# Kernel optimization log

Hardware: AMD Instinct MI355X
Metric: run time of the kernel (lower is better)

## Reference

```python
import jax, jax.numpy as jnp
import numpy as np

BLOCK_SIZE = 32
NUM_PROJS = 7


def _unit_hamming(n):
    # AngularLSH._unit_hamming_distance_array (Gray-code-like permutation)
    a = np.array([0, 1], dtype=np.int32)
    for i in range(1, n):
        a = np.concatenate([a, a[::-1] + 2 ** i])
    return a


def _lsh_hash(x, proj_dir, perm, enc_vec):
    # x: [B,H,N,D], proj_dir: [1,1,D,P] -> hash ids [B,H,N]
    pd = proj_dir[0, 0]  # [D,P]
    proj = jnp.einsum('bhnd,dp->bhnp', x, pd)
    bits = (proj > 0).astype(jnp.int32)
    bin_ids = (bits * enc_vec).sum(-1)
    return perm[bin_ids]


def _causal_attn(q, k, v):
    # q,k,v: [B,N,H,D] (xformers layout), causal softmax attention
    B, N, H, D = q.shape
    s = jnp.einsum('bqhd,bkhd->bhqk', q, k) * (D ** -0.5)
    causal = jnp.tril(jnp.ones((N, N), dtype=bool))
    s = jnp.where(causal, s, jnp.finfo(s.dtype).min)
    w = jax.nn.softmax(s, axis=-1)
    return jnp.einsum('bhqk,bkhd->bqhd', w, v)


def _forward(q, k, v, proj_dir):
    B, N, H, D = q.shape
    bs = BLOCK_SIZE
    nb = N // bs
    perm = jnp.asarray(_unit_hamming(NUM_PROJS))
    enc_vec = jnp.asarray(2 ** np.arange(NUM_PROJS, dtype=np.int32))

    qt = jnp.transpose(q, (0, 2, 1, 3))  # [B,H,N,D]
    kt = jnp.transpose(k, (0, 2, 1, 3))

    q_hash = _lsh_hash(qt, proj_dir, perm, enc_vec)  # [B,H,N]
    sort_idx = jnp.argsort(q_hash, axis=2, stable=True)
    q_hash_sort = jnp.take_along_axis(q_hash, sort_idx, axis=2)
    inv_idx = jnp.argsort(sort_idx, axis=2, stable=True)
    q_sorted = jnp.take_along_axis(qt, sort_idx[..., None], axis=2)  # [B,H,N,D]

    k_hash = _lsh_hash(kt, proj_dir, perm, enc_vec)  # [B,H,N]

    # torch .view(seq_len, -1) on [B,H,N] contiguous tensors (C-order reshape)
    qh_rows = q_hash_sort.reshape(N, -1)  # [N, B*H]
    kh_rows = k_hash.reshape(N, -1)
    eq = (qh_rows == kh_rows).reshape(nb, -1)  # rows grouped by query block
    keep = (eq.sum(axis=1) > 0)  # [nb] block kept if any hash match

    # K_split_per_block = k.reshape(B, nb, -1, D) on [B,H,N,D]
    k_blocks = kt.reshape(B, nb, (H * N) // nb, D)
    k_blocks = k_blocks * keep[None, :, None, None].astype(kt.dtype)
    k_crit = k_blocks.reshape(B, H, N, D)

    # out_critical = attn(q_critical, k_critical, v_critical) then unsort
    out = _causal_attn(jnp.transpose(q_sorted, (0, 2, 1, 3)),
                       jnp.transpose(k_crit, (0, 2, 1, 3)),
                       v)  # [B,N,H,D]
    out = jnp.take_along_axis(jnp.transpose(out, (0, 2, 1, 3)), inv_idx[..., None], axis=2)
    return jnp.transpose(out, (0, 2, 1, 3))  # [B,N,H,D]


def setup_inputs() -> dict:
    key = jax.random.key(0)
    k1, k2, k3, k4 = jax.random.split(key, 4)
    B, N, H, D = 2, 2048, 16, 128
    return {
        'q': jax.random.normal(k1, (B, N, H, D), dtype=jnp.float32),
        'k': jax.random.normal(k2, (B, N, H, D), dtype=jnp.float32),
        'v': jax.random.normal(k3, (B, N, H, D), dtype=jnp.float32),
        'proj_dir': jax.random.normal(k4, (1, 1, D, NUM_PROJS), dtype=jnp.float32),
        'is_causal': 1,
        'mask': jnp.zeros((1, 1), dtype=bool),
    }


def reference(q, k, v, proj_dir, is_causal, mask):
    # is_causal is always True at every attention call site; mask is unused then.
    return _forward(q, k, v, proj_dir)
```

## Files before the change

### kernel.cpp

```cpp
#include <hip/hip_runtime.h>
#include <cstdint>

#define BB 2
#define NN 2048
#define HH 16
#define DD 128
#define BH 32
#define NPROJ 7

typedef __bf16 bf16x8 __attribute__((ext_vector_type(8)));
typedef float f32x4 __attribute__((ext_vector_type(4)));

__device__ __forceinline__ unsigned short f2bf(float f) {
  unsigned int u = __float_as_uint(f);
  u += 0x7fff + ((u >> 16) & 1);
  return (unsigned short)(u >> 16);
}

__device__ __forceinline__ bf16x8 load_q8(const float* p) {
  float4 a = *(const float4*)p;
  float4 b = *(const float4*)(p + 4);
  unsigned short r[8] = {f2bf(a.x), f2bf(a.y), f2bf(a.z), f2bf(a.w),
                         f2bf(b.x), f2bf(b.y), f2bf(b.z), f2bf(b.w)};
  return *(bf16x8*)r;
}

__global__ void prep_kernel(const float* __restrict__ q, const float* __restrict__ k,
                            const float* __restrict__ v, const float* __restrict__ pd,
                            int* __restrict__ qh, int* __restrict__ kh,
                            unsigned short* __restrict__ Vt) {
  __shared__ __align__(16) char smem[64 * 132 * 2];
  if (blockIdx.x < 4096) {
    float* spd = (float*)smem;
    for (int i = threadIdx.x; i < DD * NPROJ; i += 256) spd[i] = pd[i];
    __syncthreads();
    long long gid = (long long)blockIdx.x * 256 + threadIdx.x;
    int part = (int)(gid & 7);
    long long row = gid >> 3;
    const long long NR = (long long)BB * NN * HH;
    int isk = row >= NR;
    long long r = isk ? row - NR : row;
    const float* src = (isk ? k : q) + r * DD + part * 16;
    double acc[NPROJ];
    for (int p = 0; p < NPROJ; ++p) acc[p] = 0.0;
    for (int d = 0; d < 16; d += 4) {
      float4 x = *(const float4*)(src + d);
      int dbase = part * 16 + d;
      for (int p = 0; p < NPROJ; ++p) {
        acc[p] += (double)x.x * (double)spd[(dbase + 0) * NPROJ + p]
                + (double)x.y * (double)spd[(dbase + 1) * NPROJ + p]
                + (double)x.z * (double)spd[(dbase + 2) * NPROJ + p]
                + (double)x.w * (double)spd[(dbase + 3) * NPROJ + p];
      }
    }
    for (int off = 1; off < 8; off <<= 1)
      for (int p = 0; p < NPROJ; ++p) acc[p] += __shfl_xor(acc[p], off);
    if (part == 0) {
      int bin = 0;
      for (int p = 0; p < NPROJ; ++p) bin |= ((int)(acc[p] > 0.0)) << p;
      int hsh = bin ^ (bin >> 1);
      int b_ = (int)(r / (NN * HH));
      int rem = (int)(r % (NN * HH));
      int n_ = rem / HH, h_ = rem % HH;
      (isk ? kh : qh)[((long long)b_ * HH + h_) * NN + n_] = hsh;
    }
  } else {
    unsigned short (*tile)[132] = (unsigned short(*)[132])smem;
    int blk = blockIdx.x - 4096;
    int bh = blk >> 5;
    int n0 = (blk & 31) * 64;
    int b = bh >> 4, h = bh & 15;
    for (int it = 0; it < 8; ++it) {
      int cid = it * 256 + threadIdx.x;
      int r = cid >> 5, d4 = (cid & 31) * 4;
      float4 x = *(const float4*)(v + (((long long)(b * NN + n0 + r) * HH + h) << 7) + d4);
      *(ushort4*)&tile[r][d4] = make_ushort4(f2bf(x.x), f2bf(x.y), f2bf(x.z), f2bf(x.w));
    }
    __syncthreads();
    for (int it = 0; it < 8; ++it) {
      int cid = it * 256 + threadIdx.x;
      int d = cid >> 4, n4 = (cid & 15) * 4;
      ushort4 y = make_ushort4(tile[n4 + 0][d], tile[n4 + 1][d], tile[n4 + 2][d], tile[n4 + 3][d]);
      *(ushort4*)(Vt + ((long long)bh * DD + d) * NN + n0 + n4) = y;
    }
  }
}

__global__ void sortkeep_kernel(const int* __restrict__ qh, const int* __restrict__ kh,
                                int* __restrict__ sidx, int* __restrict__ keep) {
  __shared__ int sh[NN];
  __shared__ int cnt[4][128];
  __shared__ int cum[128];
  __shared__ int kflag[2];
  int bh = blockIdx.x;
  const int* src = qh + (long long)bh * NN;
  for (int i = threadIdx.x; i < NN; i += 512) sh[i] = src[i];
  if (threadIdx.x < 2) kflag[threadIdx.x] = 0;
  __syncthreads();
  int bin = threadIdx.x & 127, seg = threadIdx.x >> 7;
  int n0 = seg * (NN / 4);
  int c = 0;
  for (int n = n0; n < n0 + NN / 4; ++n) c += (sh[n] == bin);
  cnt[seg][bin] = c;
  __syncthreads();
  if (threadIdx.x == 0) {
    int run = 0;
    for (int t = 0; t < 128; ++t) {
      cum[t] = run;
      run += cnt[0][t] + cnt[1][t] + cnt[2][t] + cnt[3][t];
    }
  }
  __syncthreads();
  int pos = cum[bin];
  for (int s = 0; s < seg; ++s) pos += cnt[s][bin];
  int f0 = 0, f1 = 0;
  for (int n = n0; n < n0 + NN / 4; ++n)
    if (sh[n] == bin) {
      sidx[(long long)bh * NN + pos] = n;
      int match = (bin == kh[(long long)bh * NN + pos]);
      if (pos < 1024) f0 |= match; else f1 |= match;
      ++pos;
    }
  if (f0) atomicOr(&kflag[0], 1);
  if (f1) atomicOr(&kflag[1], 1);
  __syncthreads();
  if (threadIdx.x < 2) keep[bh * 2 + threadIdx.x] = kflag[threadIdx.x];
}

__global__ __launch_bounds__(256, 1)
void flash_kernel(const float* __restrict__ q, const float* __restrict__ k,
                  const unsigned short* __restrict__ Vt, const int* __restrict__ sidx,
                  const int* __restrict__ keep, float* __restrict__ out) {
  __shared__ __align__(16) unsigned short Kt[64 * 136];
  __shared__ __align__(16) unsigned short Vs[128 * 72];
  __shared__ __align__(16) unsigned short Pb[4][16 * 72];

  int bx = blockIdx.x;
  int bh = blockIdx.y;
  int b = bh >> 4, h = bh & 15;
  int tid = threadIdx.x;
  int w = tid >> 6, lane = tid & 63;
  int l16 = lane & 15, qd = lane >> 4;

  const float* kbase = k + (long long)b * NN * HH * DD + h * DD;
  const unsigned short* Vb = Vt + (long long)bh * DD * NN;
  const float scale = 0.088388347648318447f;

  for (int ph = 0; ph < 2; ++ph) {
    int qt = ph ? bx : 31 - bx;
    int qrow = qt * 64 + w * 16 + l16;

    bf16x8 qf[4];
    {
      int nq = sidx[bh * NN + qrow];
      const float* p0 = q + (((long long)(b * NN + nq) * HH + h) << 7) + qd * 8;
#pragma unroll
      for (int c = 0; c < 4; ++c) qf[c] = load_q8(p0 + c * 32);
    }
    f32x4 o[8];
#pragma unroll
    for (int i = 0; i < 8; ++i) o[i] = (f32x4){0.f, 0.f, 0.f, 0.f};
    float m = -__builtin_inff(), l = 0.f;

    for (int kb = 0; kb <= qt; ++kb) {
      int k0 = kb * 64;
      int kp = keep[h * 4 + (k0 >> 9)];

      if (kp) {
#pragma unroll
        for (int it = 0; it < 8; ++it) {
          int cid = it * 256 + tid;
          int r = cid >> 5, d4 = (cid & 31) * 4;
          float4 x = *(const float4*)(kbase + (long long)(k0 + r) * (HH * DD) + d4);
          *(ushort4*)&Kt[r * 136 + d4] = make_ushort4(f2bf(x.x), f2bf(x.y), f2bf(x.z), f2bf(x.w));
        }
      } else {
#pragma unroll
        for (int it = 0; it < 8; ++it) {
          int cid = it * 256 + tid;
          int r = cid >> 5, d4 = (cid & 31) * 4;
          *(ushort4*)&Kt[r * 136 + d4] = make_ushort4(0, 0, 0, 0);
        }
      }
#pragma unroll
      for (int it = 0; it < 4; ++it) {
        int cid = it * 256 + tid;
        int r = cid >> 3, c8 = (cid & 7) * 8;
        *(uint4*)&Vs[r * 72 + c8] = *(const uint4*)(Vb + (long long)r * NN + k0 + c8);
      }
      __syncthreads();

      float s[16];
#pragma unroll
      for (int t = 0; t < 4; ++t) {
        f32x4 a1 = (f32x4){0.f, 0.f, 0.f, 0.f};
#pragma unroll
        for (int c = 0; c < 4; ++c) {
          bf16x8 kf = *(const bf16x8*)&Kt[(t * 16 + l16) * 136 + c * 32 + qd * 8];
          a1 = __builtin_amdgcn_mfma_f32_16x16x32_bf16(kf, qf[c], a1, 0, 0, 0);
        }
#pragma unroll
        for (int r = 0; r < 4; ++r) {
          int keyg = k0 + t * 16 + qd * 4 + r;
          s[t * 4 + r] = (keyg > qrow) ? -__builtin_inff() : a1[r] * scale;
        }
      }

      {
        float mloc = s[0];
#pragma unroll
        for (int i = 1; i < 16; ++i) mloc = fmaxf(mloc, s[i]);
        mloc = fmaxf(mloc, __shfl_xor(mloc, 16));
        mloc = fmaxf(mloc, __shfl_xor(mloc, 32));
        float mnew = fmaxf(m, mloc);
        float alpha = __expf(m - mnew);
        float psum = 0.f;
#pragma unroll
        for (int t = 0; t < 4; ++t) {
          float p0 = __expf(s[t * 4 + 0] - mnew);
          float p1 = __expf(s[t * 4 + 1] - mnew);
          float p2 = __expf(s[t * 4 + 2] - mnew);
          float p3 = __expf(s[t * 4 + 3] - mnew);
          psum += (p0 + p1) + (p2 + p3);
          *(ushort4*)&Pb[w][l16 * 72 + t * 16 + qd * 4] =
              make_ushort4(f2bf(p0), f2bf(p1), f2bf(p2), f2bf(p3));
        }
        psum += __shfl_xor(psum, 16);
        psum += __shfl_xor(psum, 32);
        l = l * alpha + psum;
        m = mnew;
        float aO[4];
#pragma unroll
        for (int r = 0; r < 4; ++r) aO[r] = __shfl(alpha, qd * 4 + r);
#pragma unroll
        for (int c8 = 0; c8 < 8; ++c8)
#pragma unroll
          for (int r = 0; r < 4; ++r) o[c8][r] *= aO[r];
      }

#pragma unroll
      for (int g = 0; g < 2; ++g) {
        bf16x8 pf = *(const bf16x8*)&Pb[w][l16 * 72 + g * 32 + qd * 8];
#pragma unroll
        for (int c8 = 0; c8 < 8; ++c8) {
          bf16x8 vf = *(const bf16x8*)&Vs[(c8 * 16 + l16) * 72 + g * 32 + qd * 8];
          o[c8] = __builtin_amdgcn_mfma_f32_16x16x32_bf16(pf, vf, o[c8], 0, 0, 0);
        }
      }
      __syncthreads();
    }

    float lO[4];
    int nO[4];
#pragma unroll
    for (int r = 0; r < 4; ++r) {
      lO[r] = __shfl(l, qd * 4 + r);
      nO[r] = sidx[(long long)bh * NN + qt * 64 + w * 16 + qd * 4 + r];
    }
#pragma unroll
    for (int r = 0; r < 4; ++r) {
      float inv = 1.f / lO[r];
      float* ob = out + (((long long)(b * NN + nO[r]) * HH + h) << 7) + l16;
#pragma unroll
      for (int c8 = 0; c8 < 8; ++c8)
        ob[c8 * 16] = o[c8][r] * inv;
    }
  }
}

extern "C" void kernel_launch(void* const* d_in, const int* in_sizes, int n_in,
                              void* d_out, int out_size, void* d_ws, size_t ws_size,
                              hipStream_t stream) {
  const float* q = (const float*)d_in[0];
  const float* k = (const float*)d_in[1];
  const float* v = (const float*)d_in[2];
  const float* pd = (const float*)d_in[3];
  float* out = (float*)d_out;
  char* ws = (char*)d_ws;
  int* qh   = (int*)(ws + 0);
  int* kh   = (int*)(ws + (1u << 18));
  int* sidx = (int*)(ws + (2u << 18));
  int* keep = (int*)(ws + 3u * (1u << 18));
  unsigned short* Vt = (unsigned short*)(ws + (2u << 20));

  prep_kernel<<<5120, 256, 0, stream>>>(q, k, v, pd, qh, kh, Vt);
  sortkeep_kernel<<<32, 512, 0, stream>>>(qh, kh, sidx, keep);
  flash_kernel<<<dim3(16, 32), 256, 0, stream>>>(q, k, Vt, sidx, keep, out);
}
```

Measured before the change: 363.1 us.

## Pre-convert K to bf16 with keep mask, split flash grid per query tile

Adds a kernel that converts K to a per-head contiguous bf16 buffer with the block keep mask already applied, so the flash kernel loads bf16 tiles with 16-byte vector copies instead of converting fp32 on every key tile. The flash grid doubles to one block per query tile (heaviest first) instead of each block processing a paired light and heavy tile. The P staging buffer now aliases K's shared memory behind an extra barrier, and softmax uses exp2 with the log2e factor folded into the scale. This adds a kernel launch, an extra K round trip through global memory, and a second barrier per key tile.

```diff
diff --git a/kernel.cpp b/kernel.cpp
--- a/kernel.cpp
+++ b/kernel.cpp
@@ -127,144 +127,148 @@
   if (threadIdx.x < 2) keep[bh * 2 + threadIdx.x] = kflag[threadIdx.x];
 }
 
+__global__ void convert_k_kernel(const float* __restrict__ k, const int* __restrict__ keep,
+                                 unsigned short* __restrict__ Kc) {
+  long long gid = (long long)blockIdx.x * 256 + threadIdx.x;
+  int row = (int)(gid >> 5);
+  int dg = (int)(gid & 31) * 4;
+  int bh = row >> 11, ki = row & 2047;
+  int b = bh >> 4, h = bh & 15;
+  int kp = keep[h * 4 + (ki >> 9)];
+  ushort4 y;
+  if (kp) {
+    float4 x = *(const float4*)(k + (((long long)(b * NN + ki) * HH + h) << 7) + dg);
+    y = make_ushort4(f2bf(x.x), f2bf(x.y), f2bf(x.z), f2bf(x.w));
+  } else {
+    y = make_ushort4(0, 0, 0, 0);
+  }
+  *(ushort4*)(Kc + (long long)row * DD + dg) = y;
+}
+
 __global__ __launch_bounds__(256, 1)
-void flash_kernel(const float* __restrict__ q, const float* __restrict__ k,
+void flash_kernel(const float* __restrict__ q, const unsigned short* __restrict__ Kc,
                   const unsigned short* __restrict__ Vt, const int* __restrict__ sidx,
-                  const int* __restrict__ keep, float* __restrict__ out) {
+                  float* __restrict__ out) {
   __shared__ __align__(16) unsigned short Kt[64 * 136];
   __shared__ __align__(16) unsigned short Vs[128 * 72];
-  __shared__ __align__(16) unsigned short Pb[4][16 * 72];
-
-  int bx = blockIdx.x;
+
+  int qt = 31 - blockIdx.x;
   int bh = blockIdx.y;
   int b = bh >> 4, h = bh & 15;
   int tid = threadIdx.x;
   int w = tid >> 6, lane = tid & 63;
   int l16 = lane & 15, qd = lane >> 4;
-
-  const float* kbase = k + (long long)b * NN * HH * DD + h * DD;
+  int qrow = qt * 64 + w * 16 + l16;
+  unsigned short* Pw = (unsigned short*)((char*)Kt + w * 2304);
+
+  const unsigned short* Kb = Kc + (long long)bh * NN * DD;
   const unsigned short* Vb = Vt + (long long)bh * DD * NN;
-  const float scale = 0.088388347648318447f;
-
-  for (int ph = 0; ph < 2; ++ph) {
-    int qt = ph ? bx : 31 - bx;
-    int qrow = qt * 64 + w * 16 + l16;
-
-    bf16x8 qf[4];
+
+  bf16x8 qf[4];
+  {
+    int nq = sidx[bh * NN + qrow];
+    const float* p0 = q + (((long long)(b * NN + nq) * HH + h) << 7) + qd * 8;
+#pragma unroll
+    for (int c = 0; c < 4; ++c) qf[c] = load_q8(p0 + c * 32);
+  }
+  f32x4 o[8];
+#pragma unroll
+  for (int i = 0; i < 8; ++i) o[i] = (f32x4){0.f, 0.f, 0.f, 0.f};
+  float m = -__builtin_inff(), l = 0.f;
+  const float sl2 = 0.088388347648318447f * 1.4426950408889634f;
+
+  for (int kb = 0; kb <= qt; ++kb) {
+    int k0 = kb * 64;
+
+#pragma unroll
+    for (int it = 0; it < 4; ++it) {
+      int chunk = it * 256 + tid;
+      int r = chunk >> 4, c8 = (chunk & 15) * 8;
+      *(uint4*)&Kt[r * 136 + c8] = *(const uint4*)(Kb + (long long)(k0 + r) * DD + c8);
+    }
+#pragma unroll
+    for (int it = 0; it < 4; ++it) {
+      int chunk = it * 256 + tid;
+      int d = chunk >> 3, c8 = (chunk & 7) * 8;
+      *(uint4*)&Vs[d * 72 + c8] = *(const uint4*)(Vb + (long long)d * NN + k0 + c8);
+    }
+    __syncthreads();
+
+    float s[16];
+#pragma unroll
+    for (int t = 0; t < 4; ++t) {
+      f32x4 a1 = (f32x4){0.f, 0.f, 0.f, 0.f};
+#pragma unroll
+      for (int c = 0; c < 4; ++c) {
+        bf16x8 kf = *(const bf16x8*)&Kt[(t * 16 + l16) * 136 + c * 32 + qd * 8];
+        a1 = __builtin_amdgcn_mfma_f32_16x16x32_bf16(kf, qf[c], a1, 0, 0, 0);
+      }
+#pragma unroll
+      for (int r = 0; r < 4; ++r) {
+        int keyg = k0 + t * 16 + qd * 4 + r;
+        s[t * 4 + r] = (keyg > qrow) ? -__builtin_inff() : a1[r] * sl2;
+      }
+    }
+    __syncthreads();
+
     {
-      int nq = sidx[bh * NN + qrow];
-      const float* p0 = q + (((long long)(b * NN + nq) * HH + h) << 7) + qd * 8;
-#pragma unroll
-      for (int c = 0; c < 4; ++c) qf[c] = load_q8(p0 + c * 32);
-    }
-    f32x4 o[8];
-#pragma unroll
-    for (int i = 0; i < 8; ++i) o[i] = (f32x4){0.f, 0.f, 0.f, 0.f};
-    float m = -__builtin_inff(), l = 0.f;
-
-    for (int kb = 0; kb <= qt; ++kb) {
-      int k0 = kb * 64;
-      int kp = keep[h * 4 + (k0 >> 9)];
-
-      if (kp) {
-#pragma unroll
-        for (int it = 0; it < 8; ++it) {
-          int cid = it * 256 + tid;
-          int r = cid >> 5, d4 = (cid & 31) * 4;
-          float4 x = *(const float4*)(kbase + (long long)(k0 + r) * (HH * DD) + d4);
-          *(ushort4*)&Kt[r * 136 + d4] = make_ushort4(f2bf(x.x), f2bf(x.y), f2bf(x.z), f2bf(x.w));
-        }
-      } else {
-#pragma unroll
-        for (int it = 0; it < 8; ++it) {
-          int cid = it * 256 + tid;
-          int r = cid >> 5, d4 = (cid & 31) * 4;
-          *(ushort4*)&Kt[r * 136 + d4] = make_ushort4(0, 0, 0, 0);
-        }
-      }
-#pragma unroll
-      for (int it = 0; it < 4; ++it) {
-        int cid = it * 256 + tid;
-        int r = cid >> 3, c8 = (cid & 7) * 8;
-        *(uint4*)&Vs[r * 72 + c8] = *(const uint4*)(Vb + (long long)r * NN + k0 + c8);
-      }
-      __syncthreads();
-
-      float s[16];
+      float mloc = s[0];
+#pragma unroll
+      for (int i = 1; i < 16; ++i) mloc = fmaxf(mloc, s[i]);
+      mloc = fmaxf(mloc, __shfl_xor(mloc, 16));
+      mloc = fmaxf(mloc, __shfl_xor(mloc, 32));
+      float mnew = fmaxf(m, mloc);
+      float alpha = __builtin_amdgcn_exp2f(m - mnew);
+      float psum = 0.f;
 #pragma unroll
       for (int t = 0; t < 4; ++t) {
-        f32x4 a1 = (f32x4){0.f, 0.f, 0.f, 0.f};
-#pragma unroll
-        for (int c = 0; c < 4; ++c) {
-          bf16x8 kf = *(const bf16x8*)&Kt[(t * 16 + l16) * 136 + c * 32 + qd * 8];
-          a1 = __builtin_amdgcn_mfma_f32_16x16x32_bf16(kf, qf[c], a1, 0, 0, 0);
-        }
-#pragma unroll
-        for (int r = 0; r < 4; ++r) {
-          int keyg = k0 + t * 16 + qd * 4 + r;
-          s[t * 4 + r] = (keyg > qrow) ? -__builtin_inff() : a1[r] * scale;
-        }
-      }
-
-      {
-        float mloc = s[0];
-#pragma unroll
-        for (int i = 1; i < 16; ++i) mloc = fmaxf(mloc, s[i]);
-        mloc = fmaxf(mloc, __shfl_xor(mloc, 16));
-        mloc = fmaxf(mloc, __shfl_xor(mloc, 32));
-        float mnew = fmaxf(m, mloc);
-        float alpha = __expf(m - mnew);
-        float psum = 0.f;
-#pragma unroll
-        for (int t = 0; t < 4; ++t) {
-          float p0 = __expf(s[t * 4 + 0] - mnew);
-          float p1 = __expf(s[t * 4 + 1] - mnew);
-          float p2 = __expf(s[t * 4 + 2] - mnew);
-          float p3 = __expf(s[t * 4 + 3] - mnew);
-          psum += (p0 + p1) + (p2 + p3);
-          *(ushort4*)&Pb[w][l16 * 72 + t * 16 + qd * 4] =
-              make_ushort4(f2bf(p0), f2bf(p1), f2bf(p2), f2bf(p3));
-        }
-        psum += __shfl_xor(psum, 16);
-        psum += __shfl_xor(psum, 32);
-        l = l * alpha + psum;
-        m = mnew;
-        float aO[4];
-#pragma unroll
-        for (int r = 0; r < 4; ++r) aO[r] = __shfl(alpha, qd * 4 + r);
-#pragma unroll
-        for (int c8 = 0; c8 < 8; ++c8)
-#pragma unroll
-          for (int r = 0; r < 4; ++r) o[c8][r] *= aO[r];
-      }
-
-#pragma unroll
-      for (int g = 0; g < 2; ++g) {
-        bf16x8 pf = *(const bf16x8*)&Pb[w][l16 * 72 + g * 32 + qd * 8];
-#pragma unroll
-        for (int c8 = 0; c8 < 8; ++c8) {
-          bf16x8 vf = *(const bf16x8*)&Vs[(c8 * 16 + l16) * 72 + g * 32 + qd * 8];
-          o[c8] = __builtin_amdgcn_mfma_f32_16x16x32_bf16(pf, vf, o[c8], 0, 0, 0);
-        }
-      }
-      __syncthreads();
-    }
-
-    float lO[4];
-    int nO[4];
-#pragma unroll
-    for (int r = 0; r < 4; ++r) {
-      lO[r] = __shfl(l, qd * 4 + r);
-      nO[r] = sidx[(long long)bh * NN + qt * 64 + w * 16 + qd * 4 + r];
-    }
-#pragma unroll
-    for (int r = 0; r < 4; ++r) {
-      float inv = 1.f / lO[r];
-      float* ob = out + (((long long)(b * NN + nO[r]) * HH + h) << 7) + l16;
+        float p0 = __builtin_amdgcn_exp2f(s[t * 4 + 0] - mnew);
+        float p1 = __builtin_amdgcn_exp2f(s[t * 4 + 1] - mnew);
+        float p2 = __builtin_amdgcn_exp2f(s[t * 4 + 2] - mnew);
+        float p3 = __builtin_amdgcn_exp2f(s[t * 4 + 3] - mnew);
+        psum += (p0 + p1) + (p2 + p3);
+        *(ushort4*)&Pw[l16 * 72 + t * 16 + qd * 4] =
+            make_ushort4(f2bf(p0), f2bf(p1), f2bf(p2), f2bf(p3));
+      }
+      psum += __shfl_xor(psum, 16);
+      psum += __shfl_xor(psum, 32);
+      l = l * alpha + psum;
+      m = mnew;
+      float aO[4];
+#pragma unroll
+      for (int r = 0; r < 4; ++r) aO[r] = __shfl(alpha, qd * 4 + r);
 #pragma unroll
       for (int c8 = 0; c8 < 8; ++c8)
-        ob[c8 * 16] = o[c8][r] * inv;
-    }
+#pragma unroll
+        for (int r = 0; r < 4; ++r) o[c8][r] *= aO[r];
+    }
+
+#pragma unroll
+    for (int g = 0; g < 2; ++g) {
+      bf16x8 pf = *(const bf16x8*)&Pw[l16 * 72 + g * 32 + qd * 8];
+#pragma unroll
+      for (int c8 = 0; c8 < 8; ++c8) {
+        bf16x8 vf = *(const bf16x8*)&Vs[(c8 * 16 + l16) * 72 + g * 32 + qd * 8];
+        o[c8] = __builtin_amdgcn_mfma_f32_16x16x32_bf16(pf, vf, o[c8], 0, 0, 0);
+      }
+    }
+    __syncthreads();
+  }
+
+  float lO[4];
+  int nO[4];
+#pragma unroll
+  for (int r = 0; r < 4; ++r) {
+    lO[r] = __shfl(l, qd * 4 + r);
+    nO[r] = sidx[(long long)bh * NN + qt * 64 + w * 16 + qd * 4 + r];
+  }
+#pragma unroll
+  for (int r = 0; r < 4; ++r) {
+    float inv = 1.f / lO[r];
+    float* ob = out + (((long long)(b * NN + nO[r]) * HH + h) << 7) + l16;
+#pragma unroll
+    for (int c8 = 0; c8 < 8; ++c8)
+      ob[c8 * 16] = o[c8][r] * inv;
   }
 }
 
@@ -281,9 +285,11 @@
   int* kh   = (int*)(ws + (1u << 18));
   int* sidx = (int*)(ws + (2u << 18));
   int* keep = (int*)(ws + 3u * (1u << 18));
-  unsigned short* Vt = (unsigned short*)(ws + (2u << 20));
+  unsigned short* Kc = (unsigned short*)(ws + (2u << 20));
+  unsigned short* Vt = (unsigned short*)(ws + (18u << 20));
 
   prep_kernel<<<5120, 256, 0, stream>>>(q, k, v, pd, qh, kh, Vt);
   sortkeep_kernel<<<32, 512, 0, stream>>>(qh, kh, sidx, keep);
-  flash_kernel<<<dim3(16, 32), 256, 0, stream>>>(q, k, Vt, sidx, keep, out);
-}
+  convert_k_kernel<<<8192, 256, 0, stream>>>(k, keep, Kc);
+  flash_kernel<<<dim3(32, 32), 256, 0, stream>>>(q, Kc, Vt, sidx, out);
+}
```

Measured after the change: 371.7 us. +2.4%, slower.
